# Optimization experiments

Measured on AMD Instinct MI355X. Metric: run time of the kernel, lower is better.

Reference implementation:

```python
import jax, jax.numpy as jnp
import numpy as np

N = 50000      # nodes
E = 800000     # edges (avg degree 16)
NFEAT = 256
NHID = 128
NCLASS = 40
NLAYERS_MID = 13  # gc2..gc14


def setup_inputs() -> dict:
    key = jax.random.key(0)
    ks = jax.random.split(key, 16)
    stdv_h = 1.0 / np.sqrt(NHID)     # GraphConvolution stdv = 1/sqrt(out_features)
    stdv_c = 1.0 / np.sqrt(NCLASS)
    u = lambda k, shape, s: jax.random.uniform(k, shape, jnp.float32, -s, s)
    return {
        "x": jax.random.normal(ks[0], (N, NFEAT), jnp.float32),
        "edge_src": jax.random.randint(ks[1], (E,), 0, N, jnp.int32),
        "edge_dst": jax.random.randint(ks[2], (E,), 0, N, jnp.int32),
        "edge_weight": jax.random.uniform(ks[3], (E,), jnp.float32),
        # skip-branch linear (self.weight / self.bias)
        "W0": u(ks[4], (NFEAT, NHID), stdv_h),
        "b0": u(ks[5], (NHID,), stdv_h),
        # gc1: nfeat -> nhid
        "W1": u(ks[6], (NFEAT, NHID), stdv_h),
        "b1": u(ks[7], (NHID,), stdv_h),
        # gc2..gc14: nhid -> nhid, stacked
        "Wmid": u(ks[8], (NLAYERS_MID, NHID, NHID), stdv_h),
        "bmid": u(ks[9], (NLAYERS_MID, NHID), stdv_h),
        # gc15: 14*nhid -> nclass
        "W15": u(ks[10], (14 * NHID, NCLASS), stdv_c),
        "b15": u(ks[11], (NCLASS,), stdv_c),
    }


def reference(x, edge_src, edge_dst, edge_weight, W0, b0, W1, b1, Wmid, bmid, W15, b15):
    n = x.shape[0]

    def gcn(h, W, b):
        # support = h @ W ; out = spmm(adj, support) + b  (adj as weighted edge list)
        support = h @ W
        msgs = support[edge_src] * edge_weight[:, None]           # [E, d]
        agg = jax.ops.segment_sum(msgs, edge_dst, num_segments=n)  # [N, d]
        return agg + b

    z = x @ W0 + b0
    x1 = jax.nn.relu(gcn(x, W1, b1)) + z

    def step(h, Wb):
        W, b = Wb
        hn = jax.nn.relu(gcn(h, W, b)) + h
        return hn, hn

    _, xs = jax.lax.scan(step, x1, (Wmid, bmid))   # xs: [13, N, NHID] = x2..x14
    all_x = jnp.concatenate([x1[None], xs], axis=0)  # [14, N, NHID] = x1..x14
    # concat order in torch code: (x14, x13, ..., x1)
    x_cat = jnp.swapaxes(all_x[::-1], 0, 1).reshape(n, 14 * NHID)
    # dropout is identity in eval mode
    x15 = gcn(x_cat, W15, b15)
    return jax.nn.log_softmax(x15, axis=1)
```

## Files before the change

### kernel.cpp

```cpp
#include <hip/hip_runtime.h>
#include <stdint.h>

#define NN 50000
#define EE 800000
#define DH 128
#define NC 40
#define KCAT (14*DH)
#define CAP 64

typedef __bf16 bf16x8 __attribute__((ext_vector_type(8)));
typedef float floatx4 __attribute__((ext_vector_type(4)));

__device__ __forceinline__ float bf2f(unsigned short u) {
  union { uint32_t i; float f; } v; v.i = ((uint32_t)u) << 16; return v.f;
}
__device__ __forceinline__ unsigned short f2bf(float f) {
  union { float f; uint32_t i; } v; v.f = f;
  uint32_t x = v.i;
  uint32_t r = (x + 0x7fffu + ((x >> 16) & 1u)) >> 16;
  return (unsigned short)r;
}

__global__ void zero_i32(int* p, int n) {
  int i = blockIdx.x * blockDim.x + threadIdx.x;
  if (i < n) p[i] = 0;
}

__global__ void detect_dtype(const unsigned short* xw, int* wildcnt) {
  int t = threadIdx.x;
  int wild = 0;
  for (int i = t; i < 4096; i += 256) {
    unsigned e = (xw[i] >> 7) & 0xFF;
    if (e >= 0x90) wild++;
  }
  if (wild) atomicAdd(wildcnt, wild);
}

__global__ void convert_f(const void* in, unsigned short* outp, int n, const int* flag) {
  bool isf32 = (*flag) > 32;
  for (int i = blockIdx.x * blockDim.x + threadIdx.x; i < n;
       i += gridDim.x * blockDim.x) {
    outp[i] = isf32 ? f2bf(((const float*)in)[i]) : ((const unsigned short*)in)[i];
  }
}

__global__ void transpose_w(const void* B, unsigned short* BT,
                            int L, int K, int M, int Mpad, const int* flag) {
  bool isf32 = (*flag) > 32;
  int total = L * Mpad * K;
  for (int idx = blockIdx.x * blockDim.x + threadIdx.x; idx < total;
       idx += gridDim.x * blockDim.x) {
    int k = idx % K;
    int n = (idx / K) % Mpad;
    int l = idx / (K * Mpad);
    unsigned short v = 0;
    if (n < M) {
      size_t si = (size_t)l * K * M + (size_t)k * M + n;
      v = isf32 ? f2bf(((const float*)B)[si]) : ((const unsigned short*)B)[si];
    }
    BT[idx] = v;
  }
}

__global__ void build_ell(const int* __restrict__ src, const int* __restrict__ dst,
                          const void* __restrict__ w,
                          int* __restrict__ cnt, int2* __restrict__ ell,
                          const int* __restrict__ flag) {
  bool isf32 = (*flag) > 32;
  int e = blockIdx.x * blockDim.x + threadIdx.x;
  if (e >= EE) return;
  int d = dst[e];
  if ((unsigned)d >= NN) return;
  int p = atomicAdd(&cnt[d], 1);
  if (p >= CAP) return;
  int s = src[e];
  float wf = isf32 ? ((const float*)w)[e] : bf2f(((const unsigned short*)w)[e]);
  if ((unsigned)s >= NN) { s = 0; wf = 0.f; }
  union { float f; int i; } wv; wv.f = wf;
  ell[(size_t)d * CAP + p] = make_int2(s, wv.i);
}

__global__ __launch_bounds__(256) void gemm_h(
    const unsigned short* __restrict__ A, int lda,
    const unsigned short* __restrict__ BT, int K,
    unsigned short* __restrict__ C, const unsigned short* __restrict__ bias) {
  __shared__ unsigned short As[128][40];
  __shared__ unsigned short Bs[128][40];
  int t = threadIdx.x;
  int wave = t >> 6, lane = t & 63;
  int wy = wave >> 1, wx = wave & 1;
  int q = lane >> 4, mn = lane & 15;
  int r0 = blockIdx.x * 128;
  floatx4 acc[4][4];
  floatx4 zf = {0.f, 0.f, 0.f, 0.f};
  #pragma unroll
  for (int i = 0; i < 4; ++i)
    #pragma unroll
    for (int j = 0; j < 4; ++j) acc[i][j] = zf;

  int arow = t >> 2;
  int akc = (t & 3) << 3;

  for (int k0 = 0; k0 < K; k0 += 32) {
    #pragma unroll
    for (int h = 0; h < 2; ++h) {
      int r = arow + h * 64;
      uint4 v = make_uint4(0, 0, 0, 0);
      if (r0 + r < NN) v = *(const uint4*)(A + (size_t)(r0 + r) * lda + k0 + akc);
      *(uint4*)(&As[r][akc]) = v;
    }
    #pragma unroll
    for (int h = 0; h < 2; ++h) {
      int n = arow + h * 64;
      uint4 v = *(const uint4*)(BT + (size_t)n * K + k0 + akc);
      *(uint4*)(&Bs[n][akc]) = v;
    }
    __syncthreads();
    bf16x8 fa[4], fb[4];
    #pragma unroll
    for (int i = 0; i < 4; ++i) fa[i] = *(const bf16x8*)(&As[wy * 64 + i * 16 + mn][q * 8]);
    #pragma unroll
    for (int j = 0; j < 4; ++j) fb[j] = *(const bf16x8*)(&Bs[wx * 64 + j * 16 + mn][q * 8]);
    #pragma unroll
    for (int i = 0; i < 4; ++i)
      #pragma unroll
      for (int j = 0; j < 4; ++j)
        acc[i][j] = __builtin_amdgcn_mfma_f32_16x16x32_bf16(fa[i], fb[j], acc[i][j], 0, 0, 0);
    __syncthreads();
  }
  #pragma unroll
  for (int i = 0; i < 4; ++i) {
    int rbase = r0 + wy * 64 + i * 16 + q * 4;
    #pragma unroll
    for (int j = 0; j < 4; ++j) {
      int col = wx * 64 + j * 16 + mn;
      float badd = bias ? bf2f(bias[col]) : 0.0f;
      #pragma unroll
      for (int rr = 0; rr < 4; ++rr) {
        int row = rbase + rr;
        if (row < NN) C[(size_t)row * 128 + col] = f2bf(acc[i][j][rr] + badd);
      }
    }
  }
}

__global__ __launch_bounds__(256) void gemm_cat(
    const unsigned short* __restrict__ A, const unsigned short* __restrict__ BT ,
    float* __restrict__ C) {
  __shared__ unsigned short As[128][40];
  __shared__ unsigned short Bs[48][40];
  int t = threadIdx.x;
  int wave = t >> 6, lane = t & 63;
  int q = lane >> 4, mn = lane & 15;
  int r0 = blockIdx.x * 128;
  floatx4 acc[2][3];
  floatx4 zf = {0.f, 0.f, 0.f, 0.f};
  #pragma unroll
  for (int i = 0; i < 2; ++i)
    #pragma unroll
    for (int j = 0; j < 3; ++j) acc[i][j] = zf;

  int arow = t >> 2;
  int akc = (t & 3) << 3;

  for (int k0 = 0; k0 < KCAT; k0 += 32) {
    #pragma unroll
    for (int h = 0; h < 2; ++h) {
      int r = arow + h * 64;
      uint4 v = make_uint4(0, 0, 0, 0);
      if (r0 + r < NN) v = *(const uint4*)(A + (size_t)(r0 + r) * KCAT + k0 + akc);
      *(uint4*)(&As[r][akc]) = v;
    }
    if (t < 192) {
      uint4 v = *(const uint4*)(BT + (size_t)arow * KCAT + k0 + akc);
      *(uint4*)(&Bs[arow][akc]) = v;
    }
    __syncthreads();
    bf16x8 fa[2], fb[3];
    #pragma unroll
    for (int i = 0; i < 2; ++i) fa[i] = *(const bf16x8*)(&As[wave * 32 + i * 16 + mn][q * 8]);
    #pragma unroll
    for (int j = 0; j < 3; ++j) fb[j] = *(const bf16x8*)(&Bs[j * 16 + mn][q * 8]);
    #pragma unroll
    for (int i = 0; i < 2; ++i)
      #pragma unroll
      for (int j = 0; j < 3; ++j)
        acc[i][j] = __builtin_amdgcn_mfma_f32_16x16x32_bf16(fa[i], fb[j], acc[i][j], 0, 0, 0);
    __syncthreads();
  }
  #pragma unroll
  for (int i = 0; i < 2; ++i) {
    int rbase = r0 + wave * 32 + i * 16 + q * 4;
    #pragma unroll
    for (int j = 0; j < 3; ++j) {
      int col = j * 16 + mn;
      #pragma unroll
      for (int rr = 0; rr < 4; ++rr) {
        int row = rbase + rr;
        if (row < NN && col < NC) C[(size_t)row * NC + col] = acc[i][j][rr];
      }
    }
  }
}

__global__ __launch_bounds__(256) void spmm_layer(
    const unsigned short* __restrict__ support, const int* __restrict__ cnt,
    const int2* __restrict__ ell, const unsigned short* __restrict__ bias,
    const unsigned short* __restrict__ res, int res_stride,
    unsigned short* __restrict__ out, int out_stride) {
  int wave = threadIdx.x >> 6, lane = threadIdx.x & 63;
  int row = blockIdx.x * 4 + wave;
  if (row >= NN) return;
  int n = cnt[row];
  if (n > CAP) n = CAP;
  int2 ev = ell[(size_t)row * CAP + lane];
  float a0 = 0.f, a1 = 0.f;
  int j = 0;
  for (; j + 8 <= n; j += 8) {
    uint32_t g[8];
    int sidx[8];
    #pragma unroll
    for (int u = 0; u < 8; ++u) sidx[u] = __shfl(ev.x, j + u);
    #pragma unroll
    for (int u = 0; u < 8; ++u)
      g[u] = *(const uint32_t*)(support + (size_t)sidx[u] * DH + 2 * lane);
    #pragma unroll
    for (int u = 0; u < 8; ++u) {
      union { int i; float f; } wv; wv.i = __shfl(ev.y, j + u);
      a0 += wv.f * bf2f((unsigned short)(g[u] & 0xffff));
      a1 += wv.f * bf2f((unsigned short)(g[u] >> 16));
    }
  }
  for (; j < n; ++j) {
    int s = __shfl(ev.x, j);
    union { int i; float f; } wv; wv.i = __shfl(ev.y, j);
    uint32_t g = *(const uint32_t*)(support + (size_t)s * DH + 2 * lane);
    a0 += wv.f * bf2f((unsigned short)(g & 0xffff));
    a1 += wv.f * bf2f((unsigned short)(g >> 16));
  }
  uint32_t bw = *(const uint32_t*)(bias + 2 * lane);
  uint32_t rw = *(const uint32_t*)(res + (size_t)row * res_stride + 2 * lane);
  float v0 = fmaxf(a0 + bf2f((unsigned short)(bw & 0xffff)), 0.f) +
             bf2f((unsigned short)(rw & 0xffff));
  float v1 = fmaxf(a1 + bf2f((unsigned short)(bw >> 16)), 0.f) +
             bf2f((unsigned short)(rw >> 16));
  uint32_t o = (uint32_t)f2bf(v0) | ((uint32_t)f2bf(v1) << 16);
  *(uint32_t*)(out + (size_t)row * out_stride + 2 * lane) = o;
}

__global__ __launch_bounds__(256) void spmm_softmax_out(
    const float* __restrict__ s15, const int* __restrict__ cnt,
    const int2* __restrict__ ell, const unsigned short* __restrict__ bias,
    float* __restrict__ out) {
  int wave = threadIdx.x >> 6, lane = threadIdx.x & 63;
  int row = blockIdx.x * 4 + wave;
  if (row >= NN) return;
  int n = cnt[row];
  if (n > CAP) n = CAP;
  int2 ev = ell[(size_t)row * CAP + lane];
  int fl = lane < NC ? lane : NC - 1;
  float acc = 0.f;
  int j = 0;
  for (; j + 4 <= n; j += 4) {
    float g[4];
    #pragma unroll
    for (int u = 0; u < 4; ++u) {
      int s = __shfl(ev.x, j + u);
      g[u] = s15[(size_t)s * NC + fl];
    }
    #pragma unroll
    for (int u = 0; u < 4; ++u) {
      union { int i; float f; } wv; wv.i = __shfl(ev.y, j + u);
      acc += wv.f * g[u];
    }
  }
  for (; j < n; ++j) {
    int s = __shfl(ev.x, j);
    union { int i; float f; } wv; wv.i = __shfl(ev.y, j);
    acc += wv.f * s15[(size_t)s * NC + fl];
  }
  acc += bf2f(bias[fl]);
  float v = (lane < NC) ? acc : -3.0e38f;
  float m = v;
  #pragma unroll
  for (int off = 32; off > 0; off >>= 1) m = fmaxf(m, __shfl_xor(m, off));
  float e = (lane < NC) ? expf(v - m) : 0.f;
  float sum = e;
  #pragma unroll
  for (int off = 32; off > 0; off >>= 1) sum += __shfl_xor(sum, off);
  if (lane < NC) out[(size_t)row * NC + lane] = v - m - logf(sum);
}

extern "C" void kernel_launch(void* const* d_in, const int* in_sizes, int n_in,
                              void* d_out, int out_size, void* d_ws, size_t ws_size,
                              hipStream_t stream) {
  const void* x   = d_in[0];
  const int* esrc = (const int*)d_in[1];
  const int* edst = (const int*)d_in[2];
  const void* ew  = d_in[3];
  const void* W0  = d_in[4];
  const void* b0  = d_in[5];
  const void* W1  = d_in[6];
  const void* b1  = d_in[7];
  const void* Wm  = d_in[8];
  const void* bm  = d_in[9];
  const void* W15 = d_in[10];
  const void* b15 = d_in[11];
  float* out = (float*)d_out;

  char* ws = (char*)d_ws;
  size_t off = 0;
  auto alloc = [&](size_t bytes) -> void* {
    void* p = ws + off;
    off = (off + bytes + 255) & ~(size_t)255;
    return p;
  };
  unsigned short* xcat = (unsigned short*)alloc((size_t)NN * KCAT * 2);
  unsigned short* xbf  = (unsigned short*)alloc((size_t)NN * 256 * 2);
  unsigned short* supp = (unsigned short*)alloc((size_t)NN * DH * 2);
  unsigned short* zbuf = (unsigned short*)alloc((size_t)NN * DH * 2);
  float* s15           = (float*)alloc((size_t)NN * NC * 4);
  int* counts          = (int*)alloc((size_t)(NN + 1) * 4);
  int2* ell            = (int2*)alloc((size_t)NN * CAP * 8);
  unsigned short* W0T  = (unsigned short*)alloc((size_t)256 * 128 * 2);
  unsigned short* W1T  = (unsigned short*)alloc((size_t)256 * 128 * 2);
  unsigned short* WmT  = (unsigned short*)alloc((size_t)13 * 128 * 128 * 2);
  unsigned short* W15T = (unsigned short*)alloc((size_t)48 * 1792 * 2);
  unsigned short* bb   = (unsigned short*)alloc((size_t)(128 + 128 + 13 * 128 + 40) * 2);
  if (off > ws_size) return;
  int* flag = counts + NN;
  unsigned short* b0b  = bb;
  unsigned short* b1b  = bb + 128;
  unsigned short* bmb  = bb + 256;
  unsigned short* b15b = bb + 256 + 13 * 128;

  zero_i32<<<197, 256, 0, stream>>>(counts, NN + 1);
  detect_dtype<<<1, 256, 0, stream>>>((const unsigned short*)x, flag);
  transpose_w<<<128, 256, 0, stream>>>(W0, W0T, 1, 256, 128, 128, flag);
  transpose_w<<<128, 256, 0, stream>>>(W1, W1T, 1, 256, 128, 128, flag);
  transpose_w<<<832, 256, 0, stream>>>(Wm, WmT, 13, 128, 128, 128, flag);
  transpose_w<<<336, 256, 0, stream>>>(W15, W15T, 1, 1792, 40, 48, flag);
  convert_f<<<2048, 256, 0, stream>>>(x, xbf, NN * 256, flag);
  convert_f<<<1, 128, 0, stream>>>(b0, b0b, 128, flag);
  convert_f<<<1, 128, 0, stream>>>(b1, b1b, 128, flag);
  convert_f<<<7, 256, 0, stream>>>(bm, bmb, 13 * 128, flag);
  convert_f<<<1, 64, 0, stream>>>(b15, b15b, 40, flag);
  build_ell<<<3125, 256, 0, stream>>>(esrc, edst, ew, counts, ell, flag);

  int gb = (NN + 127) / 128;
  int sb = (NN + 3) / 4;
  gemm_h<<<gb, 256, 0, stream>>>(xbf, 256, W0T, 256, zbuf, b0b);
  gemm_h<<<gb, 256, 0, stream>>>(xbf, 256, W1T, 256, supp, nullptr);
  spmm_layer<<<sb, 256, 0, stream>>>(supp, counts, ell, b1b, zbuf, DH,
                                     xcat + 13 * DH, KCAT);
  for (int l = 0; l < 13; ++l) {
    gemm_h<<<gb, 256, 0, stream>>>(xcat + (13 - l) * DH, KCAT, WmT + l * 128 * 128, 128,
                                   supp, nullptr);
    spmm_layer<<<sb, 256, 0, stream>>>(supp, counts, ell, bmb + l * DH,
                                       xcat + (13 - l) * DH, KCAT,
                                       xcat + (12 - l) * DH, KCAT);
  }
  gemm_cat<<<gb, 256, 0, stream>>>(xcat, W15T, s15);
  spmm_softmax_out<<<sb, 256, 0, stream>>>(s15, counts, ell, b15b, out);
}
```

Baseline: 970.2 us.

## Replace LDS-tiled GEMMs with direct-load MFMA kernels and fuse setup launches

The shared-memory tiled GEMMs are replaced by kernels that load MFMA fragments straight from global memory into registers. They use 64-row blocks, a K templated at compile time, and full unrolling, which removes the LDS staging and the barriers. Setup launches are merged: count zeroing is fused with dtype detection, the bias conversions become one kernel, and the x conversion is vectorised to four elements per thread. The SpMM gains a 16-wide gather unroll. Direct global fragment loads depend on L2 and cache reuse instead of LDS, and the larger unroll raises register pressure.

```diff
diff --git a/kernel.cpp b/kernel.cpp
--- a/kernel.cpp
+++ b/kernel.cpp
@@ -21,27 +21,53 @@
   return (unsigned short)r;
 }
 
-__global__ void zero_i32(int* p, int n) {
+__global__ void init_counts_detect(int* counts, const unsigned short* xw) {
   int i = blockIdx.x * blockDim.x + threadIdx.x;
-  if (i < n) p[i] = 0;
-}
-
-__global__ void detect_dtype(const unsigned short* xw, int* wildcnt) {
-  int t = threadIdx.x;
-  int wild = 0;
-  for (int i = t; i < 4096; i += 256) {
-    unsigned e = (xw[i] >> 7) & 0xFF;
-    if (e >= 0x90) wild++;
-  }
-  if (wild) atomicAdd(wildcnt, wild);
-}
-
-__global__ void convert_f(const void* in, unsigned short* outp, int n, const int* flag) {
+  if (i < NN) counts[i] = 0;
+  if (blockIdx.x == 0) {
+    int t = threadIdx.x;
+    int wild = 0;
+    for (int k = t; k < 4096; k += 256) {
+      unsigned e = (xw[k] >> 7) & 0xFF;
+      if (e >= 0x90) wild++;
+    }
+    __shared__ int red[256];
+    red[t] = wild;
+    __syncthreads();
+    for (int s = 128; s > 0; s >>= 1) {
+      if (t < s) red[t] += red[t + s];
+      __syncthreads();
+    }
+    if (t == 0) counts[NN] = red[0];
+  }
+}
+
+__global__ void convert_f4(const void* in, unsigned short* outp, int n4, const int* flag) {
   bool isf32 = (*flag) > 32;
-  for (int i = blockIdx.x * blockDim.x + threadIdx.x; i < n;
+  for (int i = blockIdx.x * blockDim.x + threadIdx.x; i < n4;
        i += gridDim.x * blockDim.x) {
-    outp[i] = isf32 ? f2bf(((const float*)in)[i]) : ((const unsigned short*)in)[i];
-  }
+    ushort4 o;
+    if (isf32) {
+      float4 v = ((const float4*)in)[i];
+      o.x = f2bf(v.x); o.y = f2bf(v.y); o.z = f2bf(v.z); o.w = f2bf(v.w);
+    } else {
+      o = ((const ushort4*)in)[i];
+    }
+    ((ushort4*)outp)[i] = o;
+  }
+}
+
+__global__ void convert_bias(const void* b0, const void* b1, const void* bm,
+                             const void* b15, unsigned short* bb, const int* flag) {
+  bool isf32 = (*flag) > 32;
+  int i = blockIdx.x * blockDim.x + threadIdx.x;
+  if (i >= 1960) return;
+  const void* src; int off;
+  if (i < 128)        { src = b0;  off = i; }
+  else if (i < 256)   { src = b1;  off = i - 128; }
+  else if (i < 1920)  { src = bm;  off = i - 256; }
+  else                { src = b15; off = i - 1920; }
+  bb[i] = isf32 ? f2bf(((const float*)src)[off]) : ((const unsigned short*)src)[off];
 }
 
 __global__ void transpose_w(const void* B, unsigned short* BT,
@@ -80,124 +106,121 @@
   ell[(size_t)d * CAP + p] = make_int2(s, wv.i);
 }
 
-__global__ __launch_bounds__(256) void gemm_h(
+template <int K>
+__global__ __launch_bounds__(256) void gemm_direct(
     const unsigned short* __restrict__ A, int lda,
-    const unsigned short* __restrict__ BT, int K,
-    unsigned short* __restrict__ C, const unsigned short* __restrict__ bias) {
-  __shared__ unsigned short As[128][40];
-  __shared__ unsigned short Bs[128][40];
-  int t = threadIdx.x;
-  int wave = t >> 6, lane = t & 63;
-  int wy = wave >> 1, wx = wave & 1;
-  int q = lane >> 4, mn = lane & 15;
-  int r0 = blockIdx.x * 128;
-  floatx4 acc[4][4];
-  floatx4 zf = {0.f, 0.f, 0.f, 0.f};
-  #pragma unroll
-  for (int i = 0; i < 4; ++i)
-    #pragma unroll
-    for (int j = 0; j < 4; ++j) acc[i][j] = zf;
-
-  int arow = t >> 2;
-  int akc = (t & 3) << 3;
-
-  for (int k0 = 0; k0 < K; k0 += 32) {
-    #pragma unroll
-    for (int h = 0; h < 2; ++h) {
-      int r = arow + h * 64;
-      uint4 v = make_uint4(0, 0, 0, 0);
-      if (r0 + r < NN) v = *(const uint4*)(A + (size_t)(r0 + r) * lda + k0 + akc);
-      *(uint4*)(&As[r][akc]) = v;
-    }
-    #pragma unroll
-    for (int h = 0; h < 2; ++h) {
-      int n = arow + h * 64;
-      uint4 v = *(const uint4*)(BT + (size_t)n * K + k0 + akc);
-      *(uint4*)(&Bs[n][akc]) = v;
-    }
-    __syncthreads();
-    bf16x8 fa[4], fb[4];
-    #pragma unroll
-    for (int i = 0; i < 4; ++i) fa[i] = *(const bf16x8*)(&As[wy * 64 + i * 16 + mn][q * 8]);
-    #pragma unroll
-    for (int j = 0; j < 4; ++j) fb[j] = *(const bf16x8*)(&Bs[wx * 64 + j * 16 + mn][q * 8]);
-    #pragma unroll
-    for (int i = 0; i < 4; ++i)
-      #pragma unroll
-      for (int j = 0; j < 4; ++j)
-        acc[i][j] = __builtin_amdgcn_mfma_f32_16x16x32_bf16(fa[i], fb[j], acc[i][j], 0, 0, 0);
-    __syncthreads();
-  }
-  #pragma unroll
-  for (int i = 0; i < 4; ++i) {
-    int rbase = r0 + wy * 64 + i * 16 + q * 4;
-    #pragma unroll
-    for (int j = 0; j < 4; ++j) {
-      int col = wx * 64 + j * 16 + mn;
-      float badd = bias ? bf2f(bias[col]) : 0.0f;
-      #pragma unroll
-      for (int rr = 0; rr < 4; ++rr) {
-        int row = rbase + rr;
-        if (row < NN) C[(size_t)row * 128 + col] = f2bf(acc[i][j][rr] + badd);
-      }
-    }
-  }
-}
-
-__global__ __launch_bounds__(256) void gemm_cat(
-    const unsigned short* __restrict__ A, const unsigned short* __restrict__ BT ,
-    float* __restrict__ C) {
-  __shared__ unsigned short As[128][40];
-  __shared__ unsigned short Bs[48][40];
+    const unsigned short* __restrict__ BT,
+    unsigned short* __restrict__ C, int ldc,
+    const unsigned short* __restrict__ bias) {
   int t = threadIdx.x;
   int wave = t >> 6, lane = t & 63;
   int q = lane >> 4, mn = lane & 15;
-  int r0 = blockIdx.x * 128;
-  floatx4 acc[2][3];
+  int r0 = blockIdx.x * 64;
+  int wcol = wave * 32;
+
+  const unsigned short* ap[4];
+  #pragma unroll
+  for (int i = 0; i < 4; ++i) {
+    int r = r0 + i * 16 + mn;
+    if (r >= NN) r = NN - 1;
+    ap[i] = A + (size_t)r * lda + q * 8;
+  }
+  const unsigned short* bp[2];
+  #pragma unroll
+  for (int j = 0; j < 2; ++j) bp[j] = BT + (size_t)(wcol + j * 16 + mn) * K + q * 8;
+
+  floatx4 acc[4][2];
   floatx4 zf = {0.f, 0.f, 0.f, 0.f};
   #pragma unroll
-  for (int i = 0; i < 2; ++i)
-    #pragma unroll
-    for (int j = 0; j < 3; ++j) acc[i][j] = zf;
-
-  int arow = t >> 2;
-  int akc = (t & 3) << 3;
-
-  for (int k0 = 0; k0 < KCAT; k0 += 32) {
-    #pragma unroll
-    for (int h = 0; h < 2; ++h) {
-      int r = arow + h * 64;
-      uint4 v = make_uint4(0, 0, 0, 0);
-      if (r0 + r < NN) v = *(const uint4*)(A + (size_t)(r0 + r) * KCAT + k0 + akc);
-      *(uint4*)(&As[r][akc]) = v;
-    }
-    if (t < 192) {
-      uint4 v = *(const uint4*)(BT + (size_t)arow * KCAT + k0 + akc);
-      *(uint4*)(&Bs[arow][akc]) = v;
-    }
-    __syncthreads();
-    bf16x8 fa[2], fb[3];
-    #pragma unroll
-    for (int i = 0; i < 2; ++i) fa[i] = *(const bf16x8*)(&As[wave * 32 + i * 16 + mn][q * 8]);
-    #pragma unroll
-    for (int j = 0; j < 3; ++j) fb[j] = *(const bf16x8*)(&Bs[j * 16 + mn][q * 8]);
-    #pragma unroll
-    for (int i = 0; i < 2; ++i)
-      #pragma unroll
-      for (int j = 0; j < 3; ++j)
-        acc[i][j] = __builtin_amdgcn_mfma_f32_16x16x32_bf16(fa[i], fb[j], acc[i][j], 0, 0, 0);
-    __syncthreads();
-  }
-  #pragma unroll
-  for (int i = 0; i < 2; ++i) {
-    int rbase = r0 + wave * 32 + i * 16 + q * 4;
-    #pragma unroll
-    for (int j = 0; j < 3; ++j) {
-      int col = j * 16 + mn;
+  for (int i = 0; i < 4; ++i)
+    #pragma unroll
+    for (int j = 0; j < 2; ++j) acc[i][j] = zf;
+
+  #pragma unroll
+  for (int kc = 0; kc < K; kc += 64) {
+    bf16x8 fa[4][2], fb[2][2];
+    #pragma unroll
+    for (int i = 0; i < 4; ++i)
+      #pragma unroll
+      for (int ks = 0; ks < 2; ++ks)
+        fa[i][ks] = *(const bf16x8*)(ap[i] + kc + ks * 32);
+    #pragma unroll
+    for (int j = 0; j < 2; ++j)
+      #pragma unroll
+      for (int ks = 0; ks < 2; ++ks)
+        fb[j][ks] = *(const bf16x8*)(bp[j] + kc + ks * 32);
+    #pragma unroll
+    for (int ks = 0; ks < 2; ++ks)
+      #pragma unroll
+      for (int i = 0; i < 4; ++i)
+        #pragma unroll
+        for (int j = 0; j < 2; ++j)
+          acc[i][j] = __builtin_amdgcn_mfma_f32_16x16x32_bf16(fa[i][ks], fb[j][ks],
+                                                              acc[i][j], 0, 0, 0);
+  }
+
+  #pragma unroll
+  for (int j = 0; j < 2; ++j) {
+    int col = wcol + j * 16 + mn;
+    float badd = bias ? bf2f(bias[col]) : 0.0f;
+    #pragma unroll
+    for (int i = 0; i < 4; ++i) {
+      int rbase = r0 + i * 16 + q * 4;
       #pragma unroll
       for (int rr = 0; rr < 4; ++rr) {
         int row = rbase + rr;
-        if (row < NN && col < NC) C[(size_t)row * NC + col] = acc[i][j][rr];
+        if (row < NN) C[(size_t)row * ldc + col] = f2bf(acc[i][j][rr] + badd);
+      }
+    }
+  }
+}
+
+__global__ __launch_bounds__(256) void gemm_cat_direct(
+    const unsigned short* __restrict__ A,
+    const unsigned short* __restrict__ BT,
+    float* __restrict__ C) {
+  int t = threadIdx.x;
+  int wave = t >> 6, lane = t & 63;
+  int q = lane >> 4, mn = lane & 15;
+  int r0 = blockIdx.x * 64 + wave * 16;
+  int ar = r0 + mn;
+  if (ar >= NN) ar = NN - 1;
+  const unsigned short* ap = A + (size_t)ar * KCAT + q * 8;
+  const unsigned short* bp[3];
+  #pragma unroll
+  for (int j = 0; j < 3; ++j) bp[j] = BT + (size_t)(j * 16 + mn) * KCAT + q * 8;
+
+  floatx4 acc[3];
+  floatx4 zf = {0.f, 0.f, 0.f, 0.f};
+  #pragma unroll
+  for (int j = 0; j < 3; ++j) acc[j] = zf;
+
+  #pragma unroll 2
+  for (int kc = 0; kc < KCAT; kc += 64) {
+    bf16x8 fa[2], fb[3][2];
+    #pragma unroll
+    for (int ks = 0; ks < 2; ++ks) fa[ks] = *(const bf16x8*)(ap + kc + ks * 32);
+    #pragma unroll
+    for (int j = 0; j < 3; ++j)
+      #pragma unroll
+      for (int ks = 0; ks < 2; ++ks)
+        fb[j][ks] = *(const bf16x8*)(bp[j] + kc + ks * 32);
+    #pragma unroll
+    for (int ks = 0; ks < 2; ++ks)
+      #pragma unroll
+      for (int j = 0; j < 3; ++j)
+        acc[j] = __builtin_amdgcn_mfma_f32_16x16x32_bf16(fa[ks], fb[j][ks], acc[j],
+                                                         0, 0, 0);
+  }
+
+  #pragma unroll
+  for (int j = 0; j < 3; ++j) {
+    int col = j * 16 + mn;
+    if (col < NC) {
+      #pragma unroll
+      for (int rr = 0; rr < 4; ++rr) {
+        int row = r0 + q * 4 + rr;
+        if (row < NN) C[(size_t)row * NC + col] = acc[j][rr];
       }
     }
   }
@@ -216,6 +239,21 @@
   int2 ev = ell[(size_t)row * CAP + lane];
   float a0 = 0.f, a1 = 0.f;
   int j = 0;
+  for (; j + 16 <= n; j += 16) {
+    uint32_t g[16];
+    int sidx[16];
+    #pragma unroll
+    for (int u = 0; u < 16; ++u) sidx[u] = __shfl(ev.x, j + u);
+    #pragma unroll
+    for (int u = 0; u < 16; ++u)
+      g[u] = *(const uint32_t*)(support + (size_t)sidx[u] * DH + 2 * lane);
+    #pragma unroll
+    for (int u = 0; u < 16; ++u) {
+      union { int i; float f; } wv; wv.i = __shfl(ev.y, j + u);
+      a0 += wv.f * bf2f((unsigned short)(g[u] & 0xffff));
+      a1 += wv.f * bf2f((unsigned short)(g[u] >> 16));
+    }
+  }
   for (; j + 8 <= n; j += 8) {
     uint32_t g[8];
     int sidx[8];
@@ -334,32 +372,28 @@
   unsigned short* bmb  = bb + 256;
   unsigned short* b15b = bb + 256 + 13 * 128;
 
-  zero_i32<<<197, 256, 0, stream>>>(counts, NN + 1);
-  detect_dtype<<<1, 256, 0, stream>>>((const unsigned short*)x, flag);
+  init_counts_detect<<<197, 256, 0, stream>>>(counts, (const unsigned short*)x);
   transpose_w<<<128, 256, 0, stream>>>(W0, W0T, 1, 256, 128, 128, flag);
   transpose_w<<<128, 256, 0, stream>>>(W1, W1T, 1, 256, 128, 128, flag);
   transpose_w<<<832, 256, 0, stream>>>(Wm, WmT, 13, 128, 128, 128, flag);
   transpose_w<<<336, 256, 0, stream>>>(W15, W15T, 1, 1792, 40, 48, flag);
-  convert_f<<<2048, 256, 0, stream>>>(x, xbf, NN * 256, flag);
-  convert_f<<<1, 128, 0, stream>>>(b0, b0b, 128, flag);
-  convert_f<<<1, 128, 0, stream>>>(b1, b1b, 128, flag);
-  convert_f<<<7, 256, 0, stream>>>(bm, bmb, 13 * 128, flag);
-  convert_f<<<1, 64, 0, stream>>>(b15, b15b, 40, flag);
+  convert_f4<<<2048, 256, 0, stream>>>(x, xbf, NN * 256 / 4, flag);
+  convert_bias<<<8, 256, 0, stream>>>(b0, b1, bm, b15, bb, flag);
   build_ell<<<3125, 256, 0, stream>>>(esrc, edst, ew, counts, ell, flag);
 
-  int gb = (NN + 127) / 128;
+  int gb = (NN + 63) / 64;
   int sb = (NN + 3) / 4;
-  gemm_h<<<gb, 256, 0, stream>>>(xbf, 256, W0T, 256, zbuf, b0b);
-  gemm_h<<<gb, 256, 0, stream>>>(xbf, 256, W1T, 256, supp, nullptr);
+  gemm_direct<256><<<gb, 256, 0, stream>>>(xbf, 256, W0T, zbuf, DH, b0b);
+  gemm_direct<256><<<gb, 256, 0, stream>>>(xbf, 256, W1T, supp, DH, nullptr);
   spmm_layer<<<sb, 256, 0, stream>>>(supp, counts, ell, b1b, zbuf, DH,
                                      xcat + 13 * DH, KCAT);
   for (int l = 0; l < 13; ++l) {
-    gemm_h<<<gb, 256, 0, stream>>>(xcat + (13 - l) * DH, KCAT, WmT + l * 128 * 128, 128,
-                                   supp, nullptr);
+    gemm_direct<128><<<gb, 256, 0, stream>>>(xcat + (13 - l) * DH, KCAT,
+                                             WmT + l * 128 * 128, supp, DH, nullptr);
     spmm_layer<<<sb, 256, 0, stream>>>(supp, counts, ell, bmb + l * DH,
                                        xcat + (13 - l) * DH, KCAT,
                                        xcat + (12 - l) * DH, KCAT);
   }
-  gemm_cat<<<gb, 256, 0, stream>>>(xcat, W15T, s15);
+  gemm_cat_direct<<<gb, 256, 0, stream>>>(xcat, W15T, s15);
   spmm_softmax_out<<<sb, 256, 0, stream>>>(s15, counts, ell, b15b, out);
 }
```

Result: slower. 1.093 ms (+12.7%).
